# Kernel tuning notes

Measured on AMD Instinct MI355X. Metric: run time of the kernel, lower is better.

Reference implementation:

```python
import jax, jax.numpy as jnp
import numpy as np

EMBED_DIM = 1024
PROJ_DIM = 512
NUM_HEADS = 8
HEAD_DIM = PROJ_DIM // NUM_HEADS
B, L = 2, 2048


def setup_inputs() -> dict:
    key = jax.random.key(0)
    ks = jax.random.split(key, 7)
    s = lambda d: 1.0 / np.sqrt(d)
    return {
        "x": jax.random.normal(ks[0], (B, L, EMBED_DIM), jnp.float32),
        "proj_W": jax.random.normal(ks[1], (EMBED_DIM, PROJ_DIM), jnp.float32) * s(EMBED_DIM),
        "proj_b": jax.random.normal(ks[2], (PROJ_DIM,), jnp.float32) * 0.01,
        "attn_Wq": jax.random.normal(ks[3], (PROJ_DIM, NUM_HEADS, HEAD_DIM), jnp.float32) * s(PROJ_DIM),
        "attn_Wk": jax.random.normal(ks[4], (PROJ_DIM, NUM_HEADS, HEAD_DIM), jnp.float32) * s(PROJ_DIM),
        "attn_Wv": jax.random.normal(ks[5], (PROJ_DIM, NUM_HEADS, HEAD_DIM), jnp.float32) * s(PROJ_DIM),
        "out_W": jax.random.normal(ks[6], (NUM_HEADS * HEAD_DIM, EMBED_DIM), jnp.float32) * s(NUM_HEADS * HEAD_DIM),
    }


def reference(x, proj_W, proj_b, attn_Wq, attn_Wk, attn_Wv, out_W):
    # ReLU projection: (B, L, embed_dim) -> (B, L, proj_dim)
    p = jax.nn.relu(x @ proj_W + proj_b)
    # Per-head projections: (B, L, C) x (C, H, Dh) -> (B, H, L, Dh)
    q = jnp.einsum('blc,chd->bhld', p, attn_Wq)
    k = jnp.einsum('blc,chd->bhld', p, attn_Wk)
    v = jnp.einsum('blc,chd->bhld', p, attn_Wv)
    scale = 1.0 / np.sqrt(HEAD_DIM).astype(np.float32)
    scores = jnp.einsum('bhqd,bhkd->bhqk', q, k) * scale  # (B, H, L, L)
    weights = jax.nn.softmax(scores, axis=-1)
    heads = jnp.einsum('bhqk,bhkd->bhqd', weights, v)  # (B, H, L, Dh)
    heads = heads.transpose(0, 2, 1, 3).reshape(p.shape[0], p.shape[1], NUM_HEADS * HEAD_DIM)
    return heads @ out_W  # (B, L, embed_dim)
```

## Files before the change

kernel.cpp:

```cpp
#include <hip/hip_runtime.h>
#include <math.h>

#define BATCH 2
#define SEQ 2048
#define BL (BATCH * SEQ)
#define EMBED 1024
#define PROJ 512
#define NHEADS 8
#define HDIM 64
#define QKVN (3 * PROJ)
#define KVSPLIT 4
#define KVQ (SEQ / KVSPLIT)

typedef _Float16 half8 __attribute__((ext_vector_type(8)));
typedef __fp16 fp16x2 __attribute__((ext_vector_type(2)));
typedef float floatx4 __attribute__((ext_vector_type(4)));

__global__ __launch_bounds__(256) void trconv(const float* __restrict__ src,
                                              _Float16* __restrict__ dst,
                                              int K, int N, float scale) {
    __shared__ float tile[64][65];
    const int t  = threadIdx.x;
    const int n0 = blockIdx.x * 64;
    const int k0 = blockIdx.y * 64;
    const int tx = t & 63;
    const int ty = t >> 6;
#pragma unroll
    for (int i = 0; i < 16; ++i) {
        int k = ty * 16 + i;
        tile[k][tx] = src[(size_t)(k0 + k) * N + n0 + tx];
    }
    __syncthreads();
#pragma unroll
    for (int i = 0; i < 16; ++i) {
        int n = ty * 16 + i;
        dst[(size_t)(n0 + n) * K + k0 + tx] = (_Float16)(tile[tx][n] * scale);
    }
}

__global__ __launch_bounds__(256) void trans_v(const _Float16* __restrict__ v,
                                               _Float16* __restrict__ vt) {
    __shared__ _Float16 tile[64][72];
    const int t  = threadIdx.x;
    const int t0 = blockIdx.x * 64;
    const int h  = blockIdx.y;
    const int b  = blockIdx.z;
    {
        const int r = t >> 2, c0 = (t & 3) * 16;
        const _Float16* src = v + (size_t)(b * SEQ + t0 + r) * QKVN + h * HDIM + c0;
        *reinterpret_cast<half8*>(&tile[r][c0])     = *reinterpret_cast<const half8*>(src);
        *reinterpret_cast<half8*>(&tile[r][c0 + 8]) = *reinterpret_cast<const half8*>(src + 8);
    }
    __syncthreads();
    {
        const int c = t >> 2, k0 = (t & 3) * 16;
        half8 o1, o2;
#pragma unroll
        for (int i = 0; i < 8; ++i) { o1[i] = tile[k0 + i][c]; o2[i] = tile[k0 + 8 + i][c]; }
        _Float16* dst = vt + ((size_t)(b * NHEADS + h) * HDIM + c) * SEQ + t0 + k0;
        *reinterpret_cast<half8*>(dst)     = o1;
        *reinterpret_cast<half8*>(dst + 8) = o2;
    }
}

template <int BM, int BN, int A_F32, int BIASRELU, int C_F32>
__global__ __launch_bounds__(256) void gemm_mfma(const void* __restrict__ Ap,
                                                 const _Float16* __restrict__ Bt,
                                                 const float* __restrict__ bias,
                                                 void* __restrict__ Cp,
                                                 int M, int N, int K) {
    __shared__ _Float16 Ah[BM][40];
    __shared__ _Float16 Bh[BN][40];

    constexpr int MF = BM / 32;
    constexpr int NF = BN / 32;
    constexpr int EPA = BM / 8;
    constexpr int TPA = 32 / EPA;
    constexpr int EPB = BN / 8;
    constexpr int TPB = 32 / EPB;

    const int t  = threadIdx.x;
    const int w  = t >> 6;
    const int l  = t & 63;
    const int lr = l & 15;
    const int lg = l >> 4;
    const int bm = blockIdx.y * BM;
    const int bn = blockIdx.x * BN;
    const int wr = w >> 1;
    const int wc = w & 1;

    const int ar = t / TPA, ac = (t % TPA) * EPA;
    const int br = t / TPB, bc = (t % TPB) * EPB;

    floatx4 acc[MF][NF];
#pragma unroll
    for (int i = 0; i < MF; ++i)
#pragma unroll
        for (int j = 0; j < NF; ++j) acc[i][j] = (floatx4){0.f, 0.f, 0.f, 0.f};

    float4 af[EPA / 4];
    half8  ah[EPA / 8];
    half8  bh[EPB / 8];

    const float* Af = (const float*)Ap;
    const _Float16* Ah16 = (const _Float16*)Ap;

    if (A_F32) {
#pragma unroll
        for (int i = 0; i < EPA / 4; ++i)
            af[i] = *reinterpret_cast<const float4*>(&Af[(size_t)(bm + ar) * K + ac + i * 4]);
    } else {
#pragma unroll
        for (int i = 0; i < EPA / 8; ++i)
            ah[i] = *reinterpret_cast<const half8*>(&Ah16[(size_t)(bm + ar) * K + ac + i * 8]);
    }
#pragma unroll
    for (int i = 0; i < EPB / 8; ++i)
        bh[i] = *reinterpret_cast<const half8*>(&Bt[(size_t)(bn + br) * K + bc + i * 8]);

    for (int kt = 0; kt < K; kt += 32) {
        if (A_F32) {
#pragma unroll
            for (int i = 0; i < EPA / 8; ++i) {
                half8 hcv;
                float4 a0 = af[2 * i], a1 = af[2 * i + 1];
                hcv[0] = (_Float16)a0.x; hcv[1] = (_Float16)a0.y;
                hcv[2] = (_Float16)a0.z; hcv[3] = (_Float16)a0.w;
                hcv[4] = (_Float16)a1.x; hcv[5] = (_Float16)a1.y;
                hcv[6] = (_Float16)a1.z; hcv[7] = (_Float16)a1.w;
                *reinterpret_cast<half8*>(&Ah[ar][ac + i * 8]) = hcv;
            }
        } else {
#pragma unroll
            for (int i = 0; i < EPA / 8; ++i)
                *reinterpret_cast<half8*>(&Ah[ar][ac + i * 8]) = ah[i];
        }
#pragma unroll
        for (int i = 0; i < EPB / 8; ++i)
            *reinterpret_cast<half8*>(&Bh[br][bc + i * 8]) = bh[i];
        __syncthreads();

        if (kt + 32 < K) {
            if (A_F32) {
#pragma unroll
                for (int i = 0; i < EPA / 4; ++i)
                    af[i] = *reinterpret_cast<const float4*>(&Af[(size_t)(bm + ar) * K + kt + 32 + ac + i * 4]);
            } else {
#pragma unroll
                for (int i = 0; i < EPA / 8; ++i)
                    ah[i] = *reinterpret_cast<const half8*>(&Ah16[(size_t)(bm + ar) * K + kt + 32 + ac + i * 8]);
            }
#pragma unroll
            for (int i = 0; i < EPB / 8; ++i)
                bh[i] = *reinterpret_cast<const half8*>(&Bt[(size_t)(bn + br) * K + kt + 32 + bc + i * 8]);
        }

        half8 afr[MF], bfr[NF];
#pragma unroll
        for (int mf = 0; mf < MF; ++mf)
            afr[mf] = *reinterpret_cast<const half8*>(&Ah[wr * (BM / 2) + mf * 16 + lr][lg * 8]);
#pragma unroll
        for (int nf = 0; nf < NF; ++nf)
            bfr[nf] = *reinterpret_cast<const half8*>(&Bh[wc * (BN / 2) + nf * 16 + lr][lg * 8]);
        __builtin_amdgcn_s_setprio(1);
#pragma unroll
        for (int mf = 0; mf < MF; ++mf)
#pragma unroll
            for (int nf = 0; nf < NF; ++nf)
                acc[mf][nf] = __builtin_amdgcn_mfma_f32_16x16x32_f16(afr[mf], bfr[nf], acc[mf][nf], 0, 0, 0);
        __builtin_amdgcn_s_setprio(0);

        __syncthreads();
    }

#pragma unroll
    for (int mf = 0; mf < MF; ++mf)
#pragma unroll
        for (int nf = 0; nf < NF; ++nf) {
            const int n = bn + wc * (BN / 2) + nf * 16 + lr;
            float bs = 0.f;
            if (BIASRELU) bs = bias[n];
#pragma unroll
            for (int r = 0; r < 4; ++r) {
                const int m = bm + wr * (BM / 2) + mf * 16 + lg * 4 + r;
                float v = acc[mf][nf][r];
                if (BIASRELU) v = fmaxf(v + bs, 0.f);
                if (C_F32)
                    ((float*)Cp)[(size_t)m * N + n] = v;
                else
                    ((_Float16*)Cp)[(size_t)m * N + n] = (_Float16)v;
            }
        }
}

__global__ __launch_bounds__(256) void attn_part(const _Float16* __restrict__ Q,
                                                 const _Float16* __restrict__ K,
                                                 const _Float16* __restrict__ Vt,
                                                 _Float16* __restrict__ Op,
                                                 float* __restrict__ ml) {
    __shared__ _Float16 Ks[64][72];
    __shared__ _Float16 Vs[64][72];
    __shared__ _Float16 Ps[4][16][72];

    const int t  = threadIdx.x;
    const int w  = t >> 6;
    const int l  = t & 63;
    const int lr = l & 15;
    const int lg = l >> 4;

    const int qt  = blockIdx.x >> 2;
    const int kvs = blockIdx.x & 3;
    const int q0  = qt * 64;
    const int h   = blockIdx.y;
    const int b   = blockIdx.z;
    const size_t base  = (size_t)b * SEQ * QKVN + (size_t)h * HDIM;
    const size_t vbase = (size_t)(b * NHEADS + h) * HDIM * SEQ;
    const size_t poff  = (((size_t)kvs * BATCH + b) * NHEADS + h) * SEQ;

    const int kt0  = kvs * KVQ;
    const int kend = kt0 + KVQ;

    half8 qf[2];
#pragma unroll
    for (int s = 0; s < 2; ++s) {
        const int qrow = q0 + w * 16 + lr;
        qf[s] = *reinterpret_cast<const half8*>(
            &Q[base + (size_t)qrow * QKVN + s * 32 + lg * 8]);
    }

    floatx4 o_acc[4];
#pragma unroll
    for (int j = 0; j < 4; ++j) o_acc[j] = (floatx4){0.f, 0.f, 0.f, 0.f};

    float m_s = -1e30f;
    float l_s = 0.f;

    const int rkv = t >> 2;
    const int d0  = (t & 3) * 16;

    half8 ka0, ka1, va0, va1;
    {
        const _Float16* kp = K + base + (size_t)(kt0 + rkv) * QKVN + d0;
        ka0 = *reinterpret_cast<const half8*>(kp);
        ka1 = *reinterpret_cast<const half8*>(kp + 8);
        const _Float16* vp = Vt + vbase + (size_t)rkv * SEQ + kt0 + d0;
        va0 = *reinterpret_cast<const half8*>(vp);
        va1 = *reinterpret_cast<const half8*>(vp + 8);
    }

    for (int kt = kt0; kt < kend; kt += 64) {
        *reinterpret_cast<half8*>(&Ks[rkv][d0])     = ka0;
        *reinterpret_cast<half8*>(&Ks[rkv][d0 + 8]) = ka1;
        *reinterpret_cast<half8*>(&Vs[rkv][d0])     = va0;
        *reinterpret_cast<half8*>(&Vs[rkv][d0 + 8]) = va1;
        __syncthreads();

        if (kt + 64 < kend) {
            const _Float16* kp = K + base + (size_t)(kt + 64 + rkv) * QKVN + d0;
            ka0 = *reinterpret_cast<const half8*>(kp);
            ka1 = *reinterpret_cast<const half8*>(kp + 8);
            const _Float16* vp = Vt + vbase + (size_t)rkv * SEQ + kt + 64 + d0;
            va0 = *reinterpret_cast<const half8*>(vp);
            va1 = *reinterpret_cast<const half8*>(vp + 8);
        }

        floatx4 stv[4];
#pragma unroll
        for (int i = 0; i < 4; ++i) stv[i] = (floatx4){0.f, 0.f, 0.f, 0.f};
        __builtin_amdgcn_s_setprio(1);
#pragma unroll
        for (int s = 0; s < 2; ++s)
#pragma unroll
            for (int mf = 0; mf < 4; ++mf) {
                half8 kfr = *reinterpret_cast<const half8*>(&Ks[mf * 16 + lr][s * 32 + lg * 8]);
                stv[mf] = __builtin_amdgcn_mfma_f32_16x16x32_f16(kfr, qf[s], stv[mf], 0, 0, 0);
            }
        __builtin_amdgcn_s_setprio(0);

        float tm = -1e30f;
#pragma unroll
        for (int mf = 0; mf < 4; ++mf)
#pragma unroll
            for (int r = 0; r < 4; ++r) tm = fmaxf(tm, stv[mf][r]);
        tm = fmaxf(tm, __shfl_xor(tm, 16));
        tm = fmaxf(tm, __shfl_xor(tm, 32));
        if (!__all(tm <= m_s + 8.f)) {
            float mn = fmaxf(m_s, tm);
            float fs = exp2f(m_s - mn);
            m_s = mn;
            l_s *= fs;
#pragma unroll
            for (int r = 0; r < 4; ++r) {
                float f = __shfl(fs, lg * 4 + r);
#pragma unroll
                for (int nf = 0; nf < 4; ++nf) o_acc[nf][r] *= f;
            }
        }
        float sum = 0.f;
#pragma unroll
        for (int mf = 0; mf < 4; ++mf)
#pragma unroll
            for (int r = 0; r < 4; ++r) {
                float p = exp2f(stv[mf][r] - m_s);
                stv[mf][r] = p;
                sum += p;
            }
        sum += __shfl_xor(sum, 16);
        sum += __shfl_xor(sum, 32);
        l_s += sum;

#pragma unroll
        for (int mf = 0; mf < 4; ++mf) {
            fp16x2 pk0 = __builtin_amdgcn_cvt_pkrtz(stv[mf][0], stv[mf][1]);
            fp16x2 pk1 = __builtin_amdgcn_cvt_pkrtz(stv[mf][2], stv[mf][3]);
            *reinterpret_cast<fp16x2*>(&Ps[w][lr][mf * 16 + lg * 4])     = pk0;
            *reinterpret_cast<fp16x2*>(&Ps[w][lr][mf * 16 + lg * 4 + 2]) = pk1;
        }

        __builtin_amdgcn_s_setprio(1);
#pragma unroll
        for (int s = 0; s < 2; ++s) {
            half8 pa = *reinterpret_cast<const half8*>(&Ps[w][lr][s * 32 + lg * 8]);
#pragma unroll
            for (int nf = 0; nf < 4; ++nf) {
                half8 vb = *reinterpret_cast<const half8*>(&Vs[nf * 16 + lr][s * 32 + lg * 8]);
                o_acc[nf] = __builtin_amdgcn_mfma_f32_16x16x32_f16(pa, vb, o_acc[nf], 0, 0, 0);
            }
        }
        __builtin_amdgcn_s_setprio(0);

        __syncthreads();
    }

#pragma unroll
    for (int r = 0; r < 4; ++r) {
        const int qrow = q0 + w * 16 + lg * 4 + r;
        float inv = 1.0f / __shfl(l_s, lg * 4 + r);
#pragma unroll
        for (int nf = 0; nf < 4; ++nf)
            Op[(poff + qrow) * HDIM + nf * 16 + lr] = (_Float16)(o_acc[nf][r] * inv);
    }
    if (lg == 0) {
        const int qrow = q0 + w * 16 + lr;
        reinterpret_cast<float2*>(ml)[poff + qrow] = make_float2(m_s, l_s);
    }
}

__global__ __launch_bounds__(256) void attn_merge(const _Float16* __restrict__ Op,
                                                  const float* __restrict__ ml,
                                                  _Float16* __restrict__ hd) {
    const int t  = threadIdx.x;
    const int q  = blockIdx.x * 64 + (t >> 2);
    const int d0 = (t & 3) * 16;
    const int h  = blockIdx.y;
    const int b  = blockIdx.z;

    size_t offs[KVSPLIT];
    float2 mls[KVSPLIT];
#pragma unroll
    for (int s = 0; s < KVSPLIT; ++s) {
        offs[s] = (((size_t)s * BATCH + b) * NHEADS + h) * SEQ + q;
        mls[s] = reinterpret_cast<const float2*>(ml)[offs[s]];
    }
    float m = mls[0].x;
#pragma unroll
    for (int s = 1; s < KVSPLIT; ++s) m = fmaxf(m, mls[s].x);
    float wgt[KVSPLIT];
    float wsum = 0.f;
#pragma unroll
    for (int s = 0; s < KVSPLIT; ++s) {
        wgt[s] = mls[s].y * exp2f(mls[s].x - m);
        wsum += wgt[s];
    }
    float inv = 1.0f / wsum;

    float o[16] = {};
#pragma unroll
    for (int s = 0; s < KVSPLIT; ++s) {
        const _Float16* p = Op + offs[s] * HDIM + d0;
        half8 a = *reinterpret_cast<const half8*>(p);
        half8 c = *reinterpret_cast<const half8*>(p + 8);
        float wv = wgt[s] * inv;
#pragma unroll
        for (int i = 0; i < 8; ++i) {
            o[i]     += wv * (float)a[i];
            o[8 + i] += wv * (float)c[i];
        }
    }
    half8 o0, o1;
#pragma unroll
    for (int i = 0; i < 8; ++i) { o0[i] = (_Float16)o[i]; o1[i] = (_Float16)o[8 + i]; }
    _Float16* dst = hd + (size_t)(b * SEQ + q) * PROJ + h * HDIM + d0;
    *reinterpret_cast<half8*>(dst)     = o0;
    *reinterpret_cast<half8*>(dst + 8) = o1;
}

extern "C" void kernel_launch(void* const* d_in, const int* in_sizes, int n_in,
                              void* d_out, int out_size, void* d_ws, size_t ws_size,
                              hipStream_t stream) {
    const float* x  = (const float*)d_in[0];
    const float* pW = (const float*)d_in[1];
    const float* pb = (const float*)d_in[2];
    const float* Wq = (const float*)d_in[3];
    const float* Wk = (const float*)d_in[4];
    const float* Wv = (const float*)d_in[5];
    const float* oW = (const float*)d_in[6];
    float* out = (float*)d_out;

    _Float16* ws    = (_Float16*)d_ws;
    _Float16* p_h   = ws;
    _Float16* qkv   = p_h + (size_t)BL * PROJ;
    _Float16* hd    = qkv + (size_t)BL * QKVN;
    _Float16* pWt   = hd + (size_t)BL * PROJ;
    _Float16* qkvWt = pWt + (size_t)PROJ * EMBED;
    _Float16* oWt   = qkvWt + (size_t)QKVN * PROJ;
    _Float16* vtb   = oWt + (size_t)EMBED * PROJ;
    _Float16* Oph   = vtb + (size_t)BATCH * NHEADS * HDIM * SEQ;
    float*    mlb   = (float*)(Oph + (size_t)KVSPLIT * BATCH * NHEADS * SEQ * HDIM);

    dim3 blk(256);

    trconv<<<dim3(PROJ / 64, EMBED / 64), blk, 0, stream>>>(pW, pWt, EMBED, PROJ, 1.0f);
    trconv<<<dim3(PROJ / 64, PROJ / 64), blk, 0, stream>>>(Wq, qkvWt, PROJ, PROJ, 0.125f * 1.44269504f);
    trconv<<<dim3(PROJ / 64, PROJ / 64), blk, 0, stream>>>(Wk, qkvWt + (size_t)PROJ * PROJ, PROJ, PROJ, 1.0f);
    trconv<<<dim3(PROJ / 64, PROJ / 64), blk, 0, stream>>>(Wv, qkvWt + (size_t)2 * PROJ * PROJ, PROJ, PROJ, 1.0f);
    trconv<<<dim3(EMBED / 64, PROJ / 64), blk, 0, stream>>>(oW, oWt, PROJ, EMBED, 1.0f);

    gemm_mfma<64, 64, 1, 1, 0><<<dim3(PROJ / 64, BL / 64), blk, 0, stream>>>(
        (const void*)x, pWt, pb, (void*)p_h, BL, PROJ, EMBED);

    gemm_mfma<128, 128, 0, 0, 0><<<dim3(QKVN / 128, BL / 128), blk, 0, stream>>>(
        (const void*)p_h, qkvWt, nullptr, (void*)qkv, BL, QKVN, PROJ);

    trans_v<<<dim3(SEQ / 64, NHEADS, BATCH), blk, 0, stream>>>(qkv + 2 * PROJ, vtb);

    attn_part<<<dim3((SEQ / 64) * KVSPLIT, NHEADS, BATCH), blk, 0, stream>>>(
        qkv, qkv + PROJ, vtb, Oph, mlb);
    attn_merge<<<dim3(SEQ / 64, NHEADS, BATCH), blk, 0, stream>>>(Oph, mlb, hd);

    gemm_mfma<128, 64, 0, 0, 1><<<dim3(EMBED / 64, BL / 128), blk, 0, stream>>>(
        (const void*)hd, oWt, nullptr, (void*)out, BL, EMBED, PROJ);
}
```

Measured before the change: 115.4 us.

## Switch attention to 32x32x16 MFMA with register-resident P and swizzled LDS

Rewrites the partial attention kernel to use 32x32x16 MFMA tiles, with 32 query rows per wave and 128 rows per block, which halves the grid. The probability tile now moves from the QK accumulator layout into the PV operand through cross-lane shuffles instead of a round trip through shared memory. K and V tiles are stored with an XOR swizzle in place of padding to avoid bank conflicts. Rescale factors and row sums pass through a small shared array. The aim is less LDS traffic, fewer MFMA instructions and more reuse of K/V per block, in exchange for higher register pressure and fewer blocks.

```diff
diff --git a/kernel.cpp b/kernel.cpp
--- a/kernel.cpp
+++ b/kernel.cpp
@@ -15,6 +15,7 @@
 typedef _Float16 half8 __attribute__((ext_vector_type(8)));
 typedef __fp16 fp16x2 __attribute__((ext_vector_type(2)));
 typedef float floatx4 __attribute__((ext_vector_type(4)));
+typedef float floatx16 __attribute__((ext_vector_type(16)));
 
 __global__ __launch_bounds__(256) void trconv(const float* __restrict__ src,
                                               _Float16* __restrict__ dst,
@@ -193,24 +194,24 @@
         }
 }
 
-__global__ __launch_bounds__(256) void attn_part(const _Float16* __restrict__ Q,
-                                                 const _Float16* __restrict__ K,
-                                                 const _Float16* __restrict__ Vt,
-                                                 _Float16* __restrict__ Op,
-                                                 float* __restrict__ ml) {
-    __shared__ _Float16 Ks[64][72];
-    __shared__ _Float16 Vs[64][72];
-    __shared__ _Float16 Ps[4][16][72];
+__global__ __launch_bounds__(256, 4) void attn_part(const _Float16* __restrict__ Q,
+                                                    const _Float16* __restrict__ K,
+                                                    const _Float16* __restrict__ Vt,
+                                                    _Float16* __restrict__ Op,
+                                                    float* __restrict__ ml) {
+    __shared__ _Float16 Ks[64][64];
+    __shared__ _Float16 Vs[64][64];
+    __shared__ float Fs[4][32];
 
     const int t  = threadIdx.x;
     const int w  = t >> 6;
     const int l  = t & 63;
-    const int lr = l & 15;
-    const int lg = l >> 4;
+    const int ql = l & 31;
+    const int hi = l >> 5;
 
     const int qt  = blockIdx.x >> 2;
     const int kvs = blockIdx.x & 3;
-    const int q0  = qt * 64;
+    const int q0  = qt * 128;
     const int h   = blockIdx.y;
     const int b   = blockIdx.z;
     const size_t base  = (size_t)b * SEQ * QKVN + (size_t)h * HDIM;
@@ -220,111 +221,118 @@
     const int kt0  = kvs * KVQ;
     const int kend = kt0 + KVQ;
 
-    half8 qf[2];
-#pragma unroll
-    for (int s = 0; s < 2; ++s) {
-        const int qrow = q0 + w * 16 + lr;
+    half8 qf[4];
+#pragma unroll
+    for (int s = 0; s < 4; ++s)
         qf[s] = *reinterpret_cast<const half8*>(
-            &Q[base + (size_t)qrow * QKVN + s * 32 + lg * 8]);
-    }
-
-    floatx4 o_acc[4];
-#pragma unroll
-    for (int j = 0; j < 4; ++j) o_acc[j] = (floatx4){0.f, 0.f, 0.f, 0.f};
-
-    float m_s = -1e30f;
-    float l_s = 0.f;
-
-    const int rkv = t >> 2;
-    const int d0  = (t & 3) * 16;
+            &Q[base + (size_t)(q0 + w * 32 + ql) * QKVN + s * 16 + hi * 8]);
+
+    floatx16 o0 = (floatx16)0.f, o1 = (floatx16)0.f;
+    float m_s = -1e30f, l_s = 0.f;
+
+    const int rkv  = t >> 2;
+    const int c8   = (t & 3) * 2;
+    const int swz0 = (c8 ^ (rkv & 7)) * 8;
+    const int swz1 = ((c8 + 1) ^ (rkv & 7)) * 8;
 
     half8 ka0, ka1, va0, va1;
     {
-        const _Float16* kp = K + base + (size_t)(kt0 + rkv) * QKVN + d0;
+        const _Float16* kp = K + base + (size_t)(kt0 + rkv) * QKVN + c8 * 8;
         ka0 = *reinterpret_cast<const half8*>(kp);
         ka1 = *reinterpret_cast<const half8*>(kp + 8);
-        const _Float16* vp = Vt + vbase + (size_t)rkv * SEQ + kt0 + d0;
+        const _Float16* vp = Vt + vbase + (size_t)rkv * SEQ + kt0 + c8 * 8;
         va0 = *reinterpret_cast<const half8*>(vp);
         va1 = *reinterpret_cast<const half8*>(vp + 8);
     }
 
     for (int kt = kt0; kt < kend; kt += 64) {
-        *reinterpret_cast<half8*>(&Ks[rkv][d0])     = ka0;
-        *reinterpret_cast<half8*>(&Ks[rkv][d0 + 8]) = ka1;
-        *reinterpret_cast<half8*>(&Vs[rkv][d0])     = va0;
-        *reinterpret_cast<half8*>(&Vs[rkv][d0 + 8]) = va1;
+        *reinterpret_cast<half8*>(&Ks[rkv][swz0]) = ka0;
+        *reinterpret_cast<half8*>(&Ks[rkv][swz1]) = ka1;
+        *reinterpret_cast<half8*>(&Vs[rkv][swz0]) = va0;
+        *reinterpret_cast<half8*>(&Vs[rkv][swz1]) = va1;
         __syncthreads();
 
         if (kt + 64 < kend) {
-            const _Float16* kp = K + base + (size_t)(kt + 64 + rkv) * QKVN + d0;
+            const _Float16* kp = K + base + (size_t)(kt + 64 + rkv) * QKVN + c8 * 8;
             ka0 = *reinterpret_cast<const half8*>(kp);
             ka1 = *reinterpret_cast<const half8*>(kp + 8);
-            const _Float16* vp = Vt + vbase + (size_t)rkv * SEQ + kt + 64 + d0;
+            const _Float16* vp = Vt + vbase + (size_t)rkv * SEQ + (kt + 64) + c8 * 8;
             va0 = *reinterpret_cast<const half8*>(vp);
             va1 = *reinterpret_cast<const half8*>(vp + 8);
         }
 
-        floatx4 stv[4];
-#pragma unroll
-        for (int i = 0; i < 4; ++i) stv[i] = (floatx4){0.f, 0.f, 0.f, 0.f};
+        floatx16 st0 = (floatx16)0.f, st1 = (floatx16)0.f;
         __builtin_amdgcn_s_setprio(1);
 #pragma unroll
-        for (int s = 0; s < 2; ++s)
-#pragma unroll
-            for (int mf = 0; mf < 4; ++mf) {
-                half8 kfr = *reinterpret_cast<const half8*>(&Ks[mf * 16 + lr][s * 32 + lg * 8]);
-                stv[mf] = __builtin_amdgcn_mfma_f32_16x16x32_f16(kfr, qf[s], stv[mf], 0, 0, 0);
-            }
+        for (int s = 0; s < 4; ++s) {
+            const int c0 = ((2 * s + hi) ^ (ql & 7)) * 8;
+            half8 kf0 = *reinterpret_cast<const half8*>(&Ks[ql][c0]);
+            half8 kf1 = *reinterpret_cast<const half8*>(&Ks[32 + ql][c0]);
+            st0 = __builtin_amdgcn_mfma_f32_32x32x16_f16(kf0, qf[s], st0, 0, 0, 0);
+            st1 = __builtin_amdgcn_mfma_f32_32x32x16_f16(kf1, qf[s], st1, 0, 0, 0);
+        }
         __builtin_amdgcn_s_setprio(0);
 
-        float tm = -1e30f;
-#pragma unroll
-        for (int mf = 0; mf < 4; ++mf)
-#pragma unroll
-            for (int r = 0; r < 4; ++r) tm = fmaxf(tm, stv[mf][r]);
-        tm = fmaxf(tm, __shfl_xor(tm, 16));
+        float tm = st0[0];
+#pragma unroll
+        for (int i = 1; i < 16; ++i) tm = fmaxf(tm, st0[i]);
+#pragma unroll
+        for (int i = 0; i < 16; ++i) tm = fmaxf(tm, st1[i]);
         tm = fmaxf(tm, __shfl_xor(tm, 32));
         if (!__all(tm <= m_s + 8.f)) {
             float mn = fmaxf(m_s, tm);
             float fs = exp2f(m_s - mn);
             m_s = mn;
             l_s *= fs;
-#pragma unroll
-            for (int r = 0; r < 4; ++r) {
-                float f = __shfl(fs, lg * 4 + r);
-#pragma unroll
-                for (int nf = 0; nf < 4; ++nf) o_acc[nf][r] *= f;
+            if (hi == 0) Fs[w][ql] = fs;
+#pragma unroll
+            for (int r = 0; r < 16; ++r) {
+                float f = Fs[w][(r & 3) + 8 * (r >> 2) + 4 * hi];
+                o0[r] *= f;
+                o1[r] *= f;
             }
         }
         float sum = 0.f;
 #pragma unroll
-        for (int mf = 0; mf < 4; ++mf)
-#pragma unroll
-            for (int r = 0; r < 4; ++r) {
-                float p = exp2f(stv[mf][r] - m_s);
-                stv[mf][r] = p;
-                sum += p;
-            }
-        sum += __shfl_xor(sum, 16);
+        for (int i = 0; i < 16; ++i) { float p = exp2f(st0[i] - m_s); st0[i] = p; sum += p; }
+#pragma unroll
+        for (int i = 0; i < 16; ++i) { float p = exp2f(st1[i] - m_s); st1[i] = p; sum += p; }
         sum += __shfl_xor(sum, 32);
         l_s += sum;
 
-#pragma unroll
-        for (int mf = 0; mf < 4; ++mf) {
-            fp16x2 pk0 = __builtin_amdgcn_cvt_pkrtz(stv[mf][0], stv[mf][1]);
-            fp16x2 pk1 = __builtin_amdgcn_cvt_pkrtz(stv[mf][2], stv[mf][3]);
-            *reinterpret_cast<fp16x2*>(&Ps[w][lr][mf * 16 + lg * 4])     = pk0;
-            *reinterpret_cast<fp16x2*>(&Ps[w][lr][mf * 16 + lg * 4 + 2]) = pk1;
-        }
-
         __builtin_amdgcn_s_setprio(1);
 #pragma unroll
-        for (int s = 0; s < 2; ++s) {
-            half8 pa = *reinterpret_cast<const half8*>(&Ps[w][lr][s * 32 + lg * 8]);
-#pragma unroll
-            for (int nf = 0; nf < 4; ++nf) {
-                half8 vb = *reinterpret_cast<const half8*>(&Vs[nf * 16 + lr][s * 32 + lg * 8]);
-                o_acc[nf] = __builtin_amdgcn_mfma_f32_16x16x32_f16(pa, vb, o_acc[nf], 0, 0, 0);
+        for (int tt = 0; tt < 4; ++tt) {
+            const int rb = (tt & 1) * 8;
+            float v0, v1, v2, v3, v4, v5, v6, v7;
+            if (tt < 2) {
+                v0 = st0[rb + 0]; v1 = st0[rb + 1]; v2 = st0[rb + 2]; v3 = st0[rb + 3];
+                v4 = st0[rb + 4]; v5 = st0[rb + 5]; v6 = st0[rb + 6]; v7 = st0[rb + 7];
+            } else {
+                v0 = st1[rb + 0]; v1 = st1[rb + 1]; v2 = st1[rb + 2]; v3 = st1[rb + 3];
+                v4 = st1[rb + 4]; v5 = st1[rb + 5]; v6 = st1[rb + 6]; v7 = st1[rb + 7];
+            }
+            union U { fp16x2 h; unsigned u; };
+            U ua0; ua0.h = __builtin_amdgcn_cvt_pkrtz(v0, v1);
+            U ua1; ua1.h = __builtin_amdgcn_cvt_pkrtz(v2, v3);
+            U ub0; ub0.h = __builtin_amdgcn_cvt_pkrtz(v4, v5);
+            U ub1; ub1.h = __builtin_amdgcn_cvt_pkrtz(v6, v7);
+            const unsigned pa0 = __shfl_xor(ua0.u, 32);
+            const unsigned pa1 = __shfl_xor(ua1.u, 32);
+            const unsigned pb0 = __shfl_xor(ub0.u, 32);
+            const unsigned pb1 = __shfl_xor(ub1.u, 32);
+            union A { unsigned u[4]; half8 h8; } pA;
+            pA.u[0] = hi ? pb0 : ua0.u;
+            pA.u[1] = hi ? pb1 : ua1.u;
+            pA.u[2] = hi ? ub0.u : pa0;
+            pA.u[3] = hi ? ub1.u : pa1;
+            const int cv = 2 * tt + hi;
+            {
+                const int c0 = ((cv ^ (ql & 7))) * 8;
+                half8 vb0 = *reinterpret_cast<const half8*>(&Vs[ql][c0]);
+                half8 vb1 = *reinterpret_cast<const half8*>(&Vs[32 + ql][c0]);
+                o0 = __builtin_amdgcn_mfma_f32_32x32x16_f16(pA.h8, vb0, o0, 0, 0, 0);
+                o1 = __builtin_amdgcn_mfma_f32_32x32x16_f16(pA.h8, vb1, o1, 0, 0, 0);
             }
         }
         __builtin_amdgcn_s_setprio(0);
@@ -332,16 +340,17 @@
         __syncthreads();
     }
 
-#pragma unroll
-    for (int r = 0; r < 4; ++r) {
-        const int qrow = q0 + w * 16 + lg * 4 + r;
-        float inv = 1.0f / __shfl(l_s, lg * 4 + r);
-#pragma unroll
-        for (int nf = 0; nf < 4; ++nf)
-            Op[(poff + qrow) * HDIM + nf * 16 + lr] = (_Float16)(o_acc[nf][r] * inv);
-    }
-    if (lg == 0) {
-        const int qrow = q0 + w * 16 + lr;
+    if (hi == 0) Fs[w][ql] = l_s;
+#pragma unroll
+    for (int r = 0; r < 16; ++r) {
+        const int qp = (r & 3) + 8 * (r >> 2) + 4 * hi;
+        const float inv = 1.0f / Fs[w][qp];
+        const int qrow = q0 + w * 32 + qp;
+        Op[(poff + qrow) * HDIM + ql]      = (_Float16)(o0[r] * inv);
+        Op[(poff + qrow) * HDIM + 32 + ql] = (_Float16)(o1[r] * inv);
+    }
+    if (hi == 0) {
+        const int qrow = q0 + w * 32 + ql;
         reinterpret_cast<float2*>(ml)[poff + qrow] = make_float2(m_s, l_s);
     }
 }
@@ -434,7 +443,7 @@
 
     trans_v<<<dim3(SEQ / 64, NHEADS, BATCH), blk, 0, stream>>>(qkv + 2 * PROJ, vtb);
 
-    attn_part<<<dim3((SEQ / 64) * KVSPLIT, NHEADS, BATCH), blk, 0, stream>>>(
+    attn_part<<<dim3((SEQ / 128) * KVSPLIT, NHEADS, BATCH), blk, 0, stream>>>(
         qkv, qkv + PROJ, vtb, Oph, mlb);
     attn_merge<<<dim3(SEQ / 64, NHEADS, BATCH), blk, 0, stream>>>(Oph, mlb, hd);
 
```

New measurement: 116.4 us. Within noise of the previous version (+0.9%).
